# Performance work log

Hardware: AMD Instinct MI355X
Metric: run time of the kernel (lower is better)

Reference implementation:

```python
import jax, jax.numpy as jnp
import numpy as np

N_NODES = 50000
N_EDGES = 800000
IN_DIM = 128
HIDDEN = 128
LATENT = 32
BN_EPS = 1e-5


def setup_inputs() -> dict:
    key = jax.random.key(0)
    ks = jax.random.split(key, 16)
    s = 0.05
    inp = {
        "x": jax.random.normal(ks[0], (N_NODES, IN_DIM), jnp.float32),
        "edge_index": jax.random.randint(ks[1], (2, N_EDGES), 0, N_NODES),
        "edge_weight": jax.random.uniform(ks[2], (N_EDGES,), jnp.float32),
        # GCN layer 0 and 1 weights/bias
        "W0": jax.random.normal(ks[3], (IN_DIM, HIDDEN), jnp.float32) * s,
        "b0": jnp.zeros((HIDDEN,), jnp.float32),
        "W1": jax.random.normal(ks[4], (HIDDEN, HIDDEN), jnp.float32) * s,
        "b1": jnp.zeros((HIDDEN,), jnp.float32),
        # BatchNorm affine params
        "g0": jnp.ones((HIDDEN,), jnp.float32),
        "be0": jnp.zeros((HIDDEN,), jnp.float32),
        "g1": jnp.ones((HIDDEN,), jnp.float32),
        "be1": jnp.zeros((HIDDEN,), jnp.float32),
        # mean / logstd head convs
        "Wm": jax.random.normal(ks[5], (HIDDEN, LATENT), jnp.float32) * s,
        "bm": jnp.zeros((LATENT,), jnp.float32),
        "Ws": jax.random.normal(ks[6], (HIDDEN, LATENT), jnp.float32) * s,
        "bs": jnp.zeros((LATENT,), jnp.float32),
        # reparameterisation noise (materialized for determinism)
        "eps": jax.random.normal(ks[7], (N_NODES, LATENT), jnp.float32),
    }
    return inp


def _gcn_norm(edge_index, edge_weight, n):
    # add self loops with weight 1, symmetric normalization (PyG GCNConv)
    loop = jnp.arange(n)
    src = jnp.concatenate([edge_index[0], loop])
    dst = jnp.concatenate([edge_index[1], loop])
    w = jnp.concatenate([edge_weight, jnp.ones((n,), edge_weight.dtype)])
    deg = jax.ops.segment_sum(w, dst, num_segments=n)
    dinv = jnp.where(deg > 0, jax.lax.rsqrt(deg), 0.0)
    norm = dinv[src] * w * dinv[dst]
    return src, dst, norm


def _gcn(x, W, b, src, dst, norm, n):
    h = x @ W                      # [n, out]
    msg = h[src] * norm[:, None]   # gather + scale per edge
    return jax.ops.segment_sum(msg, dst, num_segments=n) + b


def _bn(x, g, b):
    m = x.mean(axis=0)
    v = x.var(axis=0)
    return (x - m) * jax.lax.rsqrt(v + BN_EPS) * g + b


def reference(x, edge_index, edge_weight, W0, b0, W1, b1, g0, be0, g1, be1,
              Wm, bm, Ws, bs, eps):
    n = x.shape[0]
    src, dst, norm = _gcn_norm(edge_index, edge_weight, n)
    # layer 0: conv -> BN -> ReLU (dropout p=0 is identity); save residual
    h = jax.nn.relu(_bn(_gcn(x, W0, b0, src, dst, norm, n), g0, be0))
    residual = h
    # layer 1
    h = jax.nn.relu(_bn(_gcn(h, W1, b1, src, dst, norm, n), g1, be1))
    h = h + residual
    q_m = _gcn(h, Wm, bm, src, dst, norm, n)
    q_s = _gcn(h, Ws, bs, src, dst, norm, n)
    std = jax.nn.softplus(q_s) + 1e-6
    q_z = q_m + std * eps  # Normal(q_m, std).rsample()
    return (q_z, q_m, q_s)
```

## Files before the change

kernel.cpp:

```cpp
#include <hip/hip_runtime.h>
#include <hip/hip_bf16.h>
#include <hip/hip_fp16.h>
#include <math.h>


#define HID 128
#define LAT 32

typedef _Float16 f16x8 __attribute__((ext_vector_type(8)));
typedef float f32x4 __attribute__((ext_vector_type(4)));

#define LOH(u) __half2float(__ushort_as_half((unsigned short)((u) & 0xFFFFu)))
#define HIH(u) __half2float(__ushort_as_half((unsigned short)((u) >> 16)))

__device__ __forceinline__ unsigned pkh(float a, float b) {
  return (unsigned)__half_as_ushort(__float2half(a)) |
         ((unsigned)__half_as_ushort(__float2half(b)) << 16);
}


__global__ __launch_bounds__(256) void k_deg_edges(const int* __restrict__ dst,
    const float* __restrict__ w, unsigned long long* __restrict__ packed,
    unsigned short* __restrict__ rank, int E) {
  int e = blockIdx.x * 256 + threadIdx.x;
  if (e < E) {
    int d = dst[e];
    unsigned long long v =
        (1ULL << 48) | (unsigned long long)(w[e] * 16777216.0f);
    unsigned long long old = atomicAdd(&packed[d], v);
    rank[e] = (unsigned short)(old >> 48);
  }
}

#define SCH 1024

__global__ __launch_bounds__(256) void k_dinv_scan(
    const unsigned long long* __restrict__ packed, float* __restrict__ dinv,
    int* __restrict__ cnt, int* __restrict__ bsum, int n) {
  int t = threadIdx.x;
  int base = blockIdx.x * SCH + t * 4;
  int s = 0;
#pragma unroll
  for (int k = 0; k < 4; ++k) {
    int i = base + k;
    if (i < n) {
      unsigned long long p = packed[i];
      int c = (int)(p >> 48);
      cnt[i] = c;
      s += c;
      float d = (float)(p & 0xFFFFFFFFFFFFULL) * (1.0f / 16777216.0f) + 1.0f;
      dinv[i] = rsqrtf(d);
    }
  }
#pragma unroll
  for (int off = 32; off; off >>= 1) s += __shfl_down(s, off);
  __shared__ int ws[4];
  if ((t & 63) == 0) ws[t >> 6] = s;
  __syncthreads();
  if (t == 0) bsum[blockIdx.x] = ws[0] + ws[1] + ws[2] + ws[3];
}

__global__ __launch_bounds__(64) void k_scan_mid(const int* __restrict__ bsum,
    int* __restrict__ boff, int* __restrict__ off, int nb, int n) {
  int t = threadIdx.x;
  int val = (t < nb) ? bsum[t] : 0;
  int inc = val;
#pragma unroll
  for (int d = 1; d < 64; d <<= 1) {
    int u = __shfl_up(inc, d);
    if (t >= d) inc += u;
  }
  if (t < nb) boff[t] = inc - val;
  if (t == nb - 1) off[n] = inc;
}

__global__ __launch_bounds__(256) void k_scan_out(const int* __restrict__ cnt,
    const int* __restrict__ boff, int* __restrict__ off, int n) {
  int base = blockIdx.x * SCH + threadIdx.x * 4;
  int4 v = make_int4(0, 0, 0, 0);
  if (base + 3 < n) v = *(const int4*)&cnt[base];
  else {
    if (base + 0 < n) v.x = cnt[base + 0];
    if (base + 1 < n) v.y = cnt[base + 1];
    if (base + 2 < n) v.z = cnt[base + 2];
  }
  int s = v.x + v.y + v.z + v.w;
  int lane = threadIdx.x & 63, wv = threadIdx.x >> 6;
  int inc = s;
#pragma unroll
  for (int d = 1; d < 64; d <<= 1) {
    int u = __shfl_up(inc, d);
    if (lane >= d) inc += u;
  }
  __shared__ int wsum[4];
  if (lane == 63) wsum[wv] = inc;
  __syncthreads();
  int wbase = 0;
  for (int i = 0; i < wv; ++i) wbase += wsum[i];
  int ex = boff[blockIdx.x] + wbase + inc - s;
  int4 o = make_int4(ex, ex + v.x, ex + v.x + v.y, ex + v.x + v.y + v.z);
  if (base + 3 < n) {
    *(int4*)&off[base] = o;
  } else {
    if (base + 0 < n) off[base + 0] = o.x;
    if (base + 1 < n) off[base + 1] = o.y;
    if (base + 2 < n) off[base + 2] = o.z;
  }
}

__global__ __launch_bounds__(256) void k_fill(const int* __restrict__ src,
    const int* __restrict__ dst, const float* __restrict__ w,
    const float* __restrict__ dinv, const int* __restrict__ coff,
    const unsigned short* __restrict__ rank, unsigned int* __restrict__ erec,
    int E) {
  int e = blockIdx.x * 256 + threadIdx.x;
  if (e < E) {
    int s = src[e], d = dst[e];
    int p = coff[d] + (int)rank[e];
    __half u = __float2half(w[e] * dinv[s]);
    erec[p] = ((unsigned)s << 16) | (unsigned)__half_as_ushort(u);
  }
}

template <int NOUT>
__global__ __launch_bounds__(256) void k_wprep(const float* __restrict__ W,
    uint4* __restrict__ Wsw) {
  int tid = blockIdx.x * 256 + threadIdx.x;
  if (tid >= (NOUT / 16) * 4 * 64) return;
  int l = tid & 63, ks = (tid >> 6) & 3, nt = tid >> 8;
  int col = nt * 16 + (l & 15);
  int kbase = ks * 32 + (l >> 4) * 8;
  _Float16 vals[8];
#pragma unroll
  for (int i = 0; i < 8; ++i) vals[i] = (_Float16)W[(kbase + i) * NOUT + col];
  Wsw[tid] = *(uint4*)vals;
}

__global__ __launch_bounds__(256) void k_wprepc(const float* __restrict__ Wm,
    const float* __restrict__ Ws, const float* __restrict__ bm,
    const float* __restrict__ bs, uint4* __restrict__ Wsw,
    float* __restrict__ bcat) {
  int tid = blockIdx.x * 256 + threadIdx.x;
  if (tid < 64) bcat[tid] = (tid < 32) ? bm[tid] : bs[tid - 32];
  if (tid >= 4 * 4 * 64) return;
  int l = tid & 63, ks = (tid >> 6) & 3, nt = tid >> 8;
  int col = nt * 16 + (l & 15);
  int kbase = ks * 32 + (l >> 4) * 8;
  const float* Wsrc = (col < 32) ? Wm : Ws;
  int c = (col < 32) ? col : col - 32;
  _Float16 vals[8];
#pragma unroll
  for (int i = 0; i < 8; ++i) vals[i] = (_Float16)Wsrc[(kbase + i) * 32 + c];
  Wsw[tid] = *(uint4*)vals;
}


#define BM 64
template <int NOUT, int MODE>
__global__ __launch_bounds__(256) void k_gemm(const void* __restrict__ Xv,
    const uint4* __restrict__ Wsw, unsigned short* __restrict__ Y, int n,
    const float* __restrict__ stats, const float* __restrict__ g,
    const float* __restrict__ be, const uint4* __restrict__ Rres,
    uint4* __restrict__ Rout) {
  constexpr int NT = NOUT / 16;
  __shared__ _Float16 xs[BM * 128];
  __shared__ float scsh[256];
  const int t = threadIdx.x;
  const int row0 = blockIdx.x * BM;
  if (MODE >= 1) {
    if (t < 128) {
      float m = stats[t] / (float)n;
      float var = fmaxf(stats[128 + t] / (float)n - m * m, 0.f);
      float sc = g[t] * rsqrtf(var + 1e-5f);
      scsh[t] = sc;
      scsh[128 + t] = be[t] - m * sc;
    }
    __syncthreads();
  }
  for (int i = t; i < BM * 16; i += 256) {
    int r = i >> 4, cg = i & 15;
    bool valid = (row0 + r) < n;
    float f[8];
    if (MODE == 0) {
      float4 v0 = make_float4(0.f, 0.f, 0.f, 0.f), v1 = v0;
      if (valid) {
        v0 = ((const float4*)Xv)[(size_t)(row0 + r) * 32 + cg * 2];
        v1 = ((const float4*)Xv)[(size_t)(row0 + r) * 32 + cg * 2 + 1];
      }
      f[0] = v0.x; f[1] = v0.y; f[2] = v0.z; f[3] = v0.w;
      f[4] = v1.x; f[5] = v1.y; f[6] = v1.z; f[7] = v1.w;
    } else {
      uint4 h = valid ? ((const uint4*)Xv)[(size_t)(row0 + r) * 16 + cg]
                      : make_uint4(0, 0, 0, 0);
      f[0] = LOH(h.x); f[1] = HIH(h.x); f[2] = LOH(h.y); f[3] = HIH(h.y);
      f[4] = LOH(h.z); f[5] = HIH(h.z); f[6] = LOH(h.w); f[7] = HIH(h.w);
    }
    if (MODE >= 1) {
      int c0 = cg * 8;
#pragma unroll
      for (int j = 0; j < 8; ++j)
        f[j] = fmaxf(f[j] * scsh[c0 + j] + scsh[128 + c0 + j], 0.f);
      if (MODE == 2 && valid) {
        uint4 rr = Rres[(size_t)(row0 + r) * 16 + cg];
        f[0] += LOH(rr.x); f[1] += HIH(rr.x);
        f[2] += LOH(rr.y); f[3] += HIH(rr.y);
        f[4] += LOH(rr.z); f[5] += HIH(rr.z);
        f[6] += LOH(rr.w); f[7] += HIH(rr.w);
      }
    }
    uint4 pk;
    pk.x = pkh(f[0], f[1]);
    pk.y = pkh(f[2], f[3]);
    pk.z = pkh(f[4], f[5]);
    pk.w = pkh(f[6], f[7]);
    if (MODE == 1 && valid) Rout[(size_t)(row0 + r) * 16 + cg] = pk;
    *(uint4*)&xs[r * 128 + ((cg ^ (r & 15)) << 3)] = pk;
  }
  __syncthreads();

  const int lane = t & 63;
  const int wave = t >> 6;
  const int arow = wave * 16 + (lane & 15);
  f16x8 a[4];
#pragma unroll
  for (int ks = 0; ks < 4; ++ks) {
    int cg = ks * 4 + (lane >> 4);
    a[ks] = *(const f16x8*)&xs[arow * 128 + ((cg ^ (arow & 15)) << 3)];
  }
  const f16x8* Wf = (const f16x8*)Wsw;
  f32x4 acc[NT];
#pragma unroll
  for (int nt = 0; nt < NT; ++nt) acc[nt] = (f32x4)(0.f);
#pragma unroll
  for (int nt = 0; nt < NT; ++nt) {
#pragma unroll
    for (int ks = 0; ks < 4; ++ks) {
      f16x8 b = Wf[(nt * 4 + ks) * 64 + lane];
      acc[nt] = __builtin_amdgcn_mfma_f32_16x16x32_f16(a[ks], b, acc[nt], 0, 0, 0);
    }
  }
  const int rbase = row0 + wave * 16 + (lane >> 4) * 4;
  const int cbase = lane & 15;
#pragma unroll
  for (int j = 0; j < 4; ++j) {
    int row = rbase + j;
    if (row < n) {
#pragma unroll
      for (int nt = 0; nt < NT; ++nt)
        Y[(size_t)row * NOUT + nt * 16 + cbase] =
            __half_as_ushort(__float2half(acc[nt][j]));
    }
  }
}

__global__ __launch_bounds__(256) void k_propb128(const uint4* __restrict__ T,
    const float* __restrict__ dinv, const int* __restrict__ off,
    const unsigned int* __restrict__ erec, const float* __restrict__ bias,
    uint4* __restrict__ outv, int n) {
  constexpr int TPN = 16;
  int node = blockIdx.x * 16 + threadIdx.x / TPN;
  int f8 = threadIdx.x % TPN;
  if (node >= n) return;
  float di = dinv[node];
  float acc[8];
  {
    uint4 v = T[(size_t)node * TPN + f8];
    acc[0] = di * LOH(v.x); acc[1] = di * HIH(v.x);
    acc[2] = di * LOH(v.y); acc[3] = di * HIH(v.y);
    acc[4] = di * LOH(v.z); acc[5] = di * HIH(v.z);
    acc[6] = di * LOH(v.w); acc[7] = di * HIH(v.w);
  }
  int e = off[node], eend = off[node + 1];
  for (; e + 1 < eend; e += 2) {
    unsigned r0 = erec[e], r1 = erec[e + 1];
    uint4 v0 = T[(size_t)(r0 >> 16) * TPN + f8];
    uint4 v1 = T[(size_t)(r1 >> 16) * TPN + f8];
    float n0 = LOH(r0), n1 = LOH(r1);
    acc[0] = fmaf(n0, LOH(v0.x), acc[0]); acc[1] = fmaf(n0, HIH(v0.x), acc[1]);
    acc[2] = fmaf(n0, LOH(v0.y), acc[2]); acc[3] = fmaf(n0, HIH(v0.y), acc[3]);
    acc[4] = fmaf(n0, LOH(v0.z), acc[4]); acc[5] = fmaf(n0, HIH(v0.z), acc[5]);
    acc[6] = fmaf(n0, LOH(v0.w), acc[6]); acc[7] = fmaf(n0, HIH(v0.w), acc[7]);
    acc[0] = fmaf(n1, LOH(v1.x), acc[0]); acc[1] = fmaf(n1, HIH(v1.x), acc[1]);
    acc[2] = fmaf(n1, LOH(v1.y), acc[2]); acc[3] = fmaf(n1, HIH(v1.y), acc[3]);
    acc[4] = fmaf(n1, LOH(v1.z), acc[4]); acc[5] = fmaf(n1, HIH(v1.z), acc[5]);
    acc[6] = fmaf(n1, LOH(v1.w), acc[6]); acc[7] = fmaf(n1, HIH(v1.w), acc[7]);
  }
  if (e < eend) {
    unsigned r0 = erec[e];
    uint4 v0 = T[(size_t)(r0 >> 16) * TPN + f8];
    float n0 = LOH(r0);
    acc[0] = fmaf(n0, LOH(v0.x), acc[0]); acc[1] = fmaf(n0, HIH(v0.x), acc[1]);
    acc[2] = fmaf(n0, LOH(v0.y), acc[2]); acc[3] = fmaf(n0, HIH(v0.y), acc[3]);
    acc[4] = fmaf(n0, LOH(v0.z), acc[4]); acc[5] = fmaf(n0, HIH(v0.z), acc[5]);
    acc[6] = fmaf(n0, LOH(v0.w), acc[6]); acc[7] = fmaf(n0, HIH(v0.w), acc[7]);
  }
  float4 b0 = *(const float4*)&bias[f8 * 8];
  float4 b1 = *(const float4*)&bias[f8 * 8 + 4];
  uint4 pk;
  pk.x = pkh(fmaf(di, acc[0], b0.x), fmaf(di, acc[1], b0.y));
  pk.y = pkh(fmaf(di, acc[2], b0.z), fmaf(di, acc[3], b0.w));
  pk.z = pkh(fmaf(di, acc[4], b1.x), fmaf(di, acc[5], b1.y));
  pk.w = pkh(fmaf(di, acc[6], b1.z), fmaf(di, acc[7], b1.w));
  outv[(size_t)node * TPN + f8] = pk;
}

__global__ __launch_bounds__(256) void k_prop64_final(const uint4* __restrict__ T,
    const float* __restrict__ dinv, const int* __restrict__ off,
    const unsigned int* __restrict__ erec, const float* __restrict__ bias,
    const float* __restrict__ eps, float* __restrict__ out, int n) {
  constexpr int TPN = 8;
  int node = blockIdx.x * 32 + threadIdx.x / TPN;
  int f8 = threadIdx.x % TPN;
  if (node >= n) return;
  float di = dinv[node];
  float acc[8];
  {
    uint4 v = T[(size_t)node * TPN + f8];
    acc[0] = di * LOH(v.x); acc[1] = di * HIH(v.x);
    acc[2] = di * LOH(v.y); acc[3] = di * HIH(v.y);
    acc[4] = di * LOH(v.z); acc[5] = di * HIH(v.z);
    acc[6] = di * LOH(v.w); acc[7] = di * HIH(v.w);
  }
  int e = off[node], eend = off[node + 1];
  for (; e + 1 < eend; e += 2) {
    unsigned r0 = erec[e], r1 = erec[e + 1];
    uint4 v0 = T[(size_t)(r0 >> 16) * TPN + f8];
    uint4 v1 = T[(size_t)(r1 >> 16) * TPN + f8];
    float n0 = LOH(r0), n1 = LOH(r1);
    acc[0] = fmaf(n0, LOH(v0.x), acc[0]); acc[1] = fmaf(n0, HIH(v0.x), acc[1]);
    acc[2] = fmaf(n0, LOH(v0.y), acc[2]); acc[3] = fmaf(n0, HIH(v0.y), acc[3]);
    acc[4] = fmaf(n0, LOH(v0.z), acc[4]); acc[5] = fmaf(n0, HIH(v0.z), acc[5]);
    acc[6] = fmaf(n0, LOH(v0.w), acc[6]); acc[7] = fmaf(n0, HIH(v0.w), acc[7]);
    acc[0] = fmaf(n1, LOH(v1.x), acc[0]); acc[1] = fmaf(n1, HIH(v1.x), acc[1]);
    acc[2] = fmaf(n1, LOH(v1.y), acc[2]); acc[3] = fmaf(n1, HIH(v1.y), acc[3]);
    acc[4] = fmaf(n1, LOH(v1.z), acc[4]); acc[5] = fmaf(n1, HIH(v1.z), acc[5]);
    acc[6] = fmaf(n1, LOH(v1.w), acc[6]); acc[7] = fmaf(n1, HIH(v1.w), acc[7]);
  }
  if (e < eend) {
    unsigned r0 = erec[e];
    uint4 v0 = T[(size_t)(r0 >> 16) * TPN + f8];
    float n0 = LOH(r0);
    acc[0] = fmaf(n0, LOH(v0.x), acc[0]); acc[1] = fmaf(n0, HIH(v0.x), acc[1]);
    acc[2] = fmaf(n0, LOH(v0.y), acc[2]); acc[3] = fmaf(n0, HIH(v0.y), acc[3]);
    acc[4] = fmaf(n0, LOH(v0.z), acc[4]); acc[5] = fmaf(n0, HIH(v0.z), acc[5]);
    acc[6] = fmaf(n0, LOH(v0.w), acc[6]); acc[7] = fmaf(n0, HIH(v0.w), acc[7]);
  }
  float4 b0 = *(const float4*)&bias[f8 * 8];
  float4 b1 = *(const float4*)&bias[f8 * 8 + 4];
  float r[8];
  r[0] = fmaf(di, acc[0], b0.x); r[1] = fmaf(di, acc[1], b0.y);
  r[2] = fmaf(di, acc[2], b0.z); r[3] = fmaf(di, acc[3], b0.w);
  r[4] = fmaf(di, acc[4], b1.x); r[5] = fmaf(di, acc[5], b1.y);
  r[6] = fmaf(di, acc[6], b1.z); r[7] = fmaf(di, acc[7], b1.w);
  float p[8];
#pragma unroll
  for (int i = 0; i < 8; ++i) p[i] = __shfl_xor(r[i], 4);
  size_t M = (size_t)n * 32;
  if (f8 < 4) {
    int jb = f8 * 8;
    float4 e0 = *(const float4*)&eps[(size_t)node * 32 + jb];
    float4 e1 = *(const float4*)&eps[(size_t)node * 32 + jb + 4];
    float ev[8] = {e0.x, e0.y, e0.z, e0.w, e1.x, e1.y, e1.z, e1.w};
    float qz[8];
#pragma unroll
    for (int i = 0; i < 8; ++i) {
      float qs = p[i];
      float sp = fmaxf(qs, 0.f) + log1pf(expf(-fabsf(qs)));
      qz[i] = fmaf(sp + 1e-6f, ev[i], r[i]);
    }
    float* oz = &out[(size_t)node * 32 + jb];
    *(float4*)oz = make_float4(qz[0], qz[1], qz[2], qz[3]);
    *(float4*)(oz + 4) = make_float4(qz[4], qz[5], qz[6], qz[7]);
    float* om = &out[M + (size_t)node * 32 + jb];
    *(float4*)om = make_float4(r[0], r[1], r[2], r[3]);
    *(float4*)(om + 4) = make_float4(r[4], r[5], r[6], r[7]);
  } else {
    int jb = (f8 - 4) * 8;
    float* os = &out[2 * M + (size_t)node * 32 + jb];
    *(float4*)os = make_float4(r[0], r[1], r[2], r[3]);
    *(float4*)(os + 4) = make_float4(r[4], r[5], r[6], r[7]);
  }
}

__global__ __launch_bounds__(256) void k_stats(const uint4* __restrict__ X4,
    float* __restrict__ stats, int n) {
  int t = threadIdx.x;
  int chunk = t & 15;
  int sub = t >> 4;
  float s[8] = {0, 0, 0, 0, 0, 0, 0, 0};
  float s2[8] = {0, 0, 0, 0, 0, 0, 0, 0};
  for (int node = blockIdx.x * 16 + sub; node < n; node += gridDim.x * 16) {
    uint4 v = X4[(size_t)node * 16 + chunk];
    float f[8] = {LOH(v.x), HIH(v.x), LOH(v.y), HIH(v.y),
                  LOH(v.z), HIH(v.z), LOH(v.w), HIH(v.w)};
#pragma unroll
    for (int i = 0; i < 8; ++i) { s[i] += f[i]; s2[i] += f[i] * f[i]; }
  }
#pragma unroll
  for (int m = 16; m <= 32; m <<= 1) {
#pragma unroll
    for (int i = 0; i < 8; ++i) {
      s[i] += __shfl_xor(s[i], m);
      s2[i] += __shfl_xor(s2[i], m);
    }
  }
  __shared__ float red[4][16][16];
  if ((t & 48) == 0) {
    int wv = t >> 6;
#pragma unroll
    for (int i = 0; i < 8; ++i) {
      red[wv][chunk][i] = s[i];
      red[wv][chunk][8 + i] = s2[i];
    }
  }
  __syncthreads();
  int c16 = t >> 4, j = t & 15;
  float v = red[0][c16][j] + red[1][c16][j] + red[2][c16][j] + red[3][c16][j];
  int col = c16 * 8 + (j & 7);
  atomicAdd(&stats[(j < 8) ? col : 128 + col], v);
}


extern "C" void kernel_launch(void* const* d_in, const int* in_sizes, int n_in,
                              void* d_out, int out_size, void* d_ws, size_t ws_size,
                              hipStream_t stream) {
  const float* x  = (const float*)d_in[0];
  const int*   ei = (const int*)d_in[1];
  const float* ew = (const float*)d_in[2];
  const float* W0 = (const float*)d_in[3];
  const float* b0 = (const float*)d_in[4];
  const float* W1 = (const float*)d_in[5];
  const float* b1 = (const float*)d_in[6];
  const float* g0 = (const float*)d_in[7];
  const float* be0 = (const float*)d_in[8];
  const float* g1 = (const float*)d_in[9];
  const float* be1 = (const float*)d_in[10];
  const float* Wm = (const float*)d_in[11];
  const float* bm = (const float*)d_in[12];
  const float* Ws = (const float*)d_in[13];
  const float* bs = (const float*)d_in[14];
  const float* eps = (const float*)d_in[15];
  float* out = (float*)d_out;

  const int n = in_sizes[0] / HID;
  const int E = in_sizes[1] / 2;
  const int* esrc = ei;
  const int* edst = ei + E;

  char* base = (char*)d_ws;
  size_t cur = 0;
  auto alloc = [&](size_t bytes) {
    size_t o = cur;
    cur = (cur + bytes + 255) & ~(size_t)255;
    return (void*)(base + o);
  };
  unsigned long long* packed = (unsigned long long*)alloc((size_t)n * 8);
  float* dinv  = (float*)alloc((size_t)n * 4);
  int*   cnt   = (int*)alloc((size_t)n * 4);
  int*   coff  = (int*)alloc((size_t)(n + 1) * 4);
  unsigned short* rank = (unsigned short*)alloc((size_t)E * 2);
  unsigned int* erec = (unsigned int*)alloc((size_t)E * 4);
  int*   bsum  = (int*)alloc(64 * 4);
  int*   boff  = (int*)alloc(64 * 4);
  float* stats0 = (float*)alloc(256 * 4);
  float* stats1 = (float*)alloc(256 * 4);
  float* bcat  = (float*)alloc(64 * 4);
  uint4* Wsw0  = (uint4*)alloc(8 * 4 * 64 * 16);
  uint4* Wsw1  = (uint4*)alloc(8 * 4 * 64 * 16);
  uint4* Wswc  = (uint4*)alloc(4 * 4 * 64 * 16);
  unsigned short* bufA = (unsigned short*)alloc((size_t)n * 128 * 2);
  unsigned short* bufB = (unsigned short*)alloc((size_t)n * 128 * 2);
  unsigned short* bufC = (unsigned short*)alloc((size_t)n * 128 * 2);
  (void)ws_size;

  const int eb = (E + 255) / 256;
  const int gemmb = (n + BM - 1) / BM;
  const int scb = (n + SCH - 1) / SCH;

  k_wprep<128><<<8, 256, 0, stream>>>(W0, Wsw0);
  k_wprep<128><<<8, 256, 0, stream>>>(W1, Wsw1);
  k_wprepc<<<4, 256, 0, stream>>>(Wm, Ws, bm, bs, Wswc, bcat);

  hipMemsetAsync(packed, 0, (size_t)n * 8, stream);
  hipMemsetAsync(stats0, 0, 256 * 4, stream);
  hipMemsetAsync(stats1, 0, 256 * 4, stream);
  k_deg_edges<<<eb, 256, 0, stream>>>(edst, ew, packed, rank, E);
  k_dinv_scan<<<scb, 256, 0, stream>>>(packed, dinv, cnt, bsum, n);
  k_scan_mid<<<1, 64, 0, stream>>>(bsum, boff, coff, scb, n);
  k_scan_out<<<scb, 256, 0, stream>>>(cnt, boff, coff, n);
  k_fill<<<eb, 256, 0, stream>>>(esrc, edst, ew, dinv, coff, rank, erec, E);

  k_gemm<128, 0><<<gemmb, 256, 0, stream>>>(x, Wsw0, bufA, n, nullptr, nullptr,
                                            nullptr, nullptr, nullptr);
  k_propb128<<<(n + 15) / 16, 256, 0, stream>>>((const uint4*)bufA, dinv, coff,
                                                erec, b0, (uint4*)bufB, n);
  k_stats<<<128, 256, 0, stream>>>((const uint4*)bufB, stats0, n);

  k_gemm<128, 1><<<gemmb, 256, 0, stream>>>(bufB, Wsw1, bufA, n, stats0, g0, be0,
                                            nullptr, (uint4*)bufC);
  k_propb128<<<(n + 15) / 16, 256, 0, stream>>>((const uint4*)bufA, dinv, coff,
                                                erec, b1, (uint4*)bufB, n);
  k_stats<<<128, 256, 0, stream>>>((const uint4*)bufB, stats1, n);

  k_gemm<64, 2><<<gemmb, 256, 0, stream>>>(bufB, Wswc, bufA, n, stats1, g1, be1,
                                           (const uint4*)bufC, nullptr);
  k_prop64_final<<<(n + 31) / 32, 256, 0, stream>>>((const uint4*)bufA, dinv,
                                                    coff, erec, bcat, eps, out, n);
}
```

Measured before the change: 230.8 us.

## Merge degree atomics with first GEMM and fold mid-scan into scan_out

Launches the edge-degree atomic kernel and the layer-0 GEMM as one grid, with block index deciding the role, so the two independent jobs overlap and one launch is removed. The tiny single-block mid-scan kernel is removed by having every scan_out block redo the 64-entry block-sum scan itself. This cuts two kernel launches and their serialization gaps. In exchange, the fused kernel carries the GEMM's shared memory footprint for every block, including the atomic-only ones, which may limit occupancy.

```diff
diff --git a/kernel.cpp b/kernel.cpp
--- a/kernel.cpp
+++ b/kernel.cpp
@@ -19,145 +19,9 @@
 }
 
 
-__global__ __launch_bounds__(256) void k_deg_edges(const int* __restrict__ dst,
-    const float* __restrict__ w, unsigned long long* __restrict__ packed,
-    unsigned short* __restrict__ rank, int E) {
-  int e = blockIdx.x * 256 + threadIdx.x;
-  if (e < E) {
-    int d = dst[e];
-    unsigned long long v =
-        (1ULL << 48) | (unsigned long long)(w[e] * 16777216.0f);
-    unsigned long long old = atomicAdd(&packed[d], v);
-    rank[e] = (unsigned short)(old >> 48);
-  }
-}
-
-#define SCH 1024
-
-__global__ __launch_bounds__(256) void k_dinv_scan(
-    const unsigned long long* __restrict__ packed, float* __restrict__ dinv,
-    int* __restrict__ cnt, int* __restrict__ bsum, int n) {
-  int t = threadIdx.x;
-  int base = blockIdx.x * SCH + t * 4;
-  int s = 0;
-#pragma unroll
-  for (int k = 0; k < 4; ++k) {
-    int i = base + k;
-    if (i < n) {
-      unsigned long long p = packed[i];
-      int c = (int)(p >> 48);
-      cnt[i] = c;
-      s += c;
-      float d = (float)(p & 0xFFFFFFFFFFFFULL) * (1.0f / 16777216.0f) + 1.0f;
-      dinv[i] = rsqrtf(d);
-    }
-  }
-#pragma unroll
-  for (int off = 32; off; off >>= 1) s += __shfl_down(s, off);
-  __shared__ int ws[4];
-  if ((t & 63) == 0) ws[t >> 6] = s;
-  __syncthreads();
-  if (t == 0) bsum[blockIdx.x] = ws[0] + ws[1] + ws[2] + ws[3];
-}
-
-__global__ __launch_bounds__(64) void k_scan_mid(const int* __restrict__ bsum,
-    int* __restrict__ boff, int* __restrict__ off, int nb, int n) {
-  int t = threadIdx.x;
-  int val = (t < nb) ? bsum[t] : 0;
-  int inc = val;
-#pragma unroll
-  for (int d = 1; d < 64; d <<= 1) {
-    int u = __shfl_up(inc, d);
-    if (t >= d) inc += u;
-  }
-  if (t < nb) boff[t] = inc - val;
-  if (t == nb - 1) off[n] = inc;
-}
-
-__global__ __launch_bounds__(256) void k_scan_out(const int* __restrict__ cnt,
-    const int* __restrict__ boff, int* __restrict__ off, int n) {
-  int base = blockIdx.x * SCH + threadIdx.x * 4;
-  int4 v = make_int4(0, 0, 0, 0);
-  if (base + 3 < n) v = *(const int4*)&cnt[base];
-  else {
-    if (base + 0 < n) v.x = cnt[base + 0];
-    if (base + 1 < n) v.y = cnt[base + 1];
-    if (base + 2 < n) v.z = cnt[base + 2];
-  }
-  int s = v.x + v.y + v.z + v.w;
-  int lane = threadIdx.x & 63, wv = threadIdx.x >> 6;
-  int inc = s;
-#pragma unroll
-  for (int d = 1; d < 64; d <<= 1) {
-    int u = __shfl_up(inc, d);
-    if (lane >= d) inc += u;
-  }
-  __shared__ int wsum[4];
-  if (lane == 63) wsum[wv] = inc;
-  __syncthreads();
-  int wbase = 0;
-  for (int i = 0; i < wv; ++i) wbase += wsum[i];
-  int ex = boff[blockIdx.x] + wbase + inc - s;
-  int4 o = make_int4(ex, ex + v.x, ex + v.x + v.y, ex + v.x + v.y + v.z);
-  if (base + 3 < n) {
-    *(int4*)&off[base] = o;
-  } else {
-    if (base + 0 < n) off[base + 0] = o.x;
-    if (base + 1 < n) off[base + 1] = o.y;
-    if (base + 2 < n) off[base + 2] = o.z;
-  }
-}
-
-__global__ __launch_bounds__(256) void k_fill(const int* __restrict__ src,
-    const int* __restrict__ dst, const float* __restrict__ w,
-    const float* __restrict__ dinv, const int* __restrict__ coff,
-    const unsigned short* __restrict__ rank, unsigned int* __restrict__ erec,
-    int E) {
-  int e = blockIdx.x * 256 + threadIdx.x;
-  if (e < E) {
-    int s = src[e], d = dst[e];
-    int p = coff[d] + (int)rank[e];
-    __half u = __float2half(w[e] * dinv[s]);
-    erec[p] = ((unsigned)s << 16) | (unsigned)__half_as_ushort(u);
-  }
-}
-
-template <int NOUT>
-__global__ __launch_bounds__(256) void k_wprep(const float* __restrict__ W,
-    uint4* __restrict__ Wsw) {
-  int tid = blockIdx.x * 256 + threadIdx.x;
-  if (tid >= (NOUT / 16) * 4 * 64) return;
-  int l = tid & 63, ks = (tid >> 6) & 3, nt = tid >> 8;
-  int col = nt * 16 + (l & 15);
-  int kbase = ks * 32 + (l >> 4) * 8;
-  _Float16 vals[8];
-#pragma unroll
-  for (int i = 0; i < 8; ++i) vals[i] = (_Float16)W[(kbase + i) * NOUT + col];
-  Wsw[tid] = *(uint4*)vals;
-}
-
-__global__ __launch_bounds__(256) void k_wprepc(const float* __restrict__ Wm,
-    const float* __restrict__ Ws, const float* __restrict__ bm,
-    const float* __restrict__ bs, uint4* __restrict__ Wsw,
-    float* __restrict__ bcat) {
-  int tid = blockIdx.x * 256 + threadIdx.x;
-  if (tid < 64) bcat[tid] = (tid < 32) ? bm[tid] : bs[tid - 32];
-  if (tid >= 4 * 4 * 64) return;
-  int l = tid & 63, ks = (tid >> 6) & 3, nt = tid >> 8;
-  int col = nt * 16 + (l & 15);
-  int kbase = ks * 32 + (l >> 4) * 8;
-  const float* Wsrc = (col < 32) ? Wm : Ws;
-  int c = (col < 32) ? col : col - 32;
-  _Float16 vals[8];
-#pragma unroll
-  for (int i = 0; i < 8; ++i) vals[i] = (_Float16)Wsrc[(kbase + i) * 32 + c];
-  Wsw[tid] = *(uint4*)vals;
-}
-
-
 #define BM 64
 template <int NOUT, int MODE>
-__global__ __launch_bounds__(256) void k_gemm(const void* __restrict__ Xv,
+__device__ __forceinline__ void gemm_dev(int bid, const void* __restrict__ Xv,
     const uint4* __restrict__ Wsw, unsigned short* __restrict__ Y, int n,
     const float* __restrict__ stats, const float* __restrict__ g,
     const float* __restrict__ be, const uint4* __restrict__ Rres,
@@ -166,7 +30,7 @@
   __shared__ _Float16 xs[BM * 128];
   __shared__ float scsh[256];
   const int t = threadIdx.x;
-  const int row0 = blockIdx.x * BM;
+  const int row0 = bid * BM;
   if (MODE >= 1) {
     if (t < 128) {
       float m = stats[t] / (float)n;
@@ -251,6 +115,160 @@
             __half_as_ushort(__float2half(acc[nt][j]));
     }
   }
+}
+
+__global__ __launch_bounds__(256) void k_front(const int* __restrict__ dst,
+    const float* __restrict__ w, unsigned long long* __restrict__ packed,
+    unsigned short* __restrict__ rank, int E, int eb,
+    const float* __restrict__ x, const uint4* __restrict__ Wsw0,
+    unsigned short* __restrict__ bufA, int n) {
+  int b = blockIdx.x;
+  if (b < eb) {
+    int e = b * 256 + threadIdx.x;
+    if (e < E) {
+      int d = dst[e];
+      unsigned long long v =
+          (1ULL << 48) | (unsigned long long)(w[e] * 16777216.0f);
+      unsigned long long old = atomicAdd(&packed[d], v);
+      rank[e] = (unsigned short)(old >> 48);
+    }
+  } else {
+    gemm_dev<128, 0>(b - eb, x, Wsw0, bufA, n, nullptr, nullptr, nullptr,
+                     nullptr, nullptr);
+  }
+}
+
+template <int NOUT, int MODE>
+__global__ __launch_bounds__(256) void k_gemm(const void* __restrict__ Xv,
+    const uint4* __restrict__ Wsw, unsigned short* __restrict__ Y, int n,
+    const float* __restrict__ stats, const float* __restrict__ g,
+    const float* __restrict__ be, const uint4* __restrict__ Rres,
+    uint4* __restrict__ Rout) {
+  gemm_dev<NOUT, MODE>(blockIdx.x, Xv, Wsw, Y, n, stats, g, be, Rres, Rout);
+}
+
+#define SCH 1024
+
+__global__ __launch_bounds__(256) void k_dinv_scan(
+    const unsigned long long* __restrict__ packed, float* __restrict__ dinv,
+    int* __restrict__ cnt, int* __restrict__ bsum, int n) {
+  int t = threadIdx.x;
+  int base = blockIdx.x * SCH + t * 4;
+  int s = 0;
+#pragma unroll
+  for (int k = 0; k < 4; ++k) {
+    int i = base + k;
+    if (i < n) {
+      unsigned long long p = packed[i];
+      int c = (int)(p >> 48);
+      cnt[i] = c;
+      s += c;
+      float d = (float)(p & 0xFFFFFFFFFFFFULL) * (1.0f / 16777216.0f) + 1.0f;
+      dinv[i] = rsqrtf(d);
+    }
+  }
+#pragma unroll
+  for (int off = 32; off; off >>= 1) s += __shfl_down(s, off);
+  __shared__ int ws[4];
+  if ((t & 63) == 0) ws[t >> 6] = s;
+  __syncthreads();
+  if (t == 0) bsum[blockIdx.x] = ws[0] + ws[1] + ws[2] + ws[3];
+}
+
+__global__ __launch_bounds__(256) void k_scan_out(const int* __restrict__ cnt,
+    const int* __restrict__ bsum, int* __restrict__ off, int nb, int n) {
+  __shared__ int sboff;
+  int t = threadIdx.x;
+  if (t < 64) {
+    int val = (t < nb) ? bsum[t] : 0;
+    int inc = val;
+#pragma unroll
+    for (int d = 1; d < 64; d <<= 1) {
+      int u = __shfl_up(inc, d);
+      if (t >= d) inc += u;
+    }
+    int exc = inc - val;
+    if (t == (int)blockIdx.x) sboff = exc;
+    if (blockIdx.x == 0 && t == nb - 1) off[n] = inc;
+  }
+  __syncthreads();
+  int boff0 = sboff;
+  int base = blockIdx.x * SCH + t * 4;
+  int4 v = make_int4(0, 0, 0, 0);
+  if (base + 3 < n) v = *(const int4*)&cnt[base];
+  else {
+    if (base + 0 < n) v.x = cnt[base + 0];
+    if (base + 1 < n) v.y = cnt[base + 1];
+    if (base + 2 < n) v.z = cnt[base + 2];
+  }
+  int s = v.x + v.y + v.z + v.w;
+  int lane = t & 63, wv = t >> 6;
+  int inc = s;
+#pragma unroll
+  for (int d = 1; d < 64; d <<= 1) {
+    int u = __shfl_up(inc, d);
+    if (lane >= d) inc += u;
+  }
+  __shared__ int wsum[4];
+  if (lane == 63) wsum[wv] = inc;
+  __syncthreads();
+  int wbase = 0;
+  for (int i = 0; i < wv; ++i) wbase += wsum[i];
+  int ex = boff0 + wbase + inc - s;
+  int4 o = make_int4(ex, ex + v.x, ex + v.x + v.y, ex + v.x + v.y + v.z);
+  if (base + 3 < n) {
+    *(int4*)&off[base] = o;
+  } else {
+    if (base + 0 < n) off[base + 0] = o.x;
+    if (base + 1 < n) off[base + 1] = o.y;
+    if (base + 2 < n) off[base + 2] = o.z;
+  }
+}
+
+__global__ __launch_bounds__(256) void k_fill(const int* __restrict__ src,
+    const int* __restrict__ dst, const float* __restrict__ w,
+    const float* __restrict__ dinv, const int* __restrict__ coff,
+    const unsigned short* __restrict__ rank, unsigned int* __restrict__ erec,
+    int E) {
+  int e = blockIdx.x * 256 + threadIdx.x;
+  if (e < E) {
+    int s = src[e], d = dst[e];
+    int p = coff[d] + (int)rank[e];
+    __half u = __float2half(w[e] * dinv[s]);
+    erec[p] = ((unsigned)s << 16) | (unsigned)__half_as_ushort(u);
+  }
+}
+
+template <int NOUT>
+__global__ __launch_bounds__(256) void k_wprep(const float* __restrict__ W,
+    uint4* __restrict__ Wsw) {
+  int tid = blockIdx.x * 256 + threadIdx.x;
+  if (tid >= (NOUT / 16) * 4 * 64) return;
+  int l = tid & 63, ks = (tid >> 6) & 3, nt = tid >> 8;
+  int col = nt * 16 + (l & 15);
+  int kbase = ks * 32 + (l >> 4) * 8;
+  _Float16 vals[8];
+#pragma unroll
+  for (int i = 0; i < 8; ++i) vals[i] = (_Float16)W[(kbase + i) * NOUT + col];
+  Wsw[tid] = *(uint4*)vals;
+}
+
+__global__ __launch_bounds__(256) void k_wprepc(const float* __restrict__ Wm,
+    const float* __restrict__ Ws, const float* __restrict__ bm,
+    const float* __restrict__ bs, uint4* __restrict__ Wsw,
+    float* __restrict__ bcat) {
+  int tid = blockIdx.x * 256 + threadIdx.x;
+  if (tid < 64) bcat[tid] = (tid < 32) ? bm[tid] : bs[tid - 32];
+  if (tid >= 4 * 4 * 64) return;
+  int l = tid & 63, ks = (tid >> 6) & 3, nt = tid >> 8;
+  int col = nt * 16 + (l & 15);
+  int kbase = ks * 32 + (l >> 4) * 8;
+  const float* Wsrc = (col < 32) ? Wm : Ws;
+  int c = (col < 32) ? col : col - 32;
+  _Float16 vals[8];
+#pragma unroll
+  for (int i = 0; i < 8; ++i) vals[i] = (_Float16)Wsrc[(kbase + i) * 32 + c];
+  Wsw[tid] = *(uint4*)vals;
 }
 
 __global__ __launch_bounds__(256) void k_propb128(const uint4* __restrict__ T,
@@ -461,7 +479,6 @@
   unsigned short* rank = (unsigned short*)alloc((size_t)E * 2);
   unsigned int* erec = (unsigned int*)alloc((size_t)E * 4);
   int*   bsum  = (int*)alloc(64 * 4);
-  int*   boff  = (int*)alloc(64 * 4);
   float* stats0 = (float*)alloc(256 * 4);
   float* stats1 = (float*)alloc(256 * 4);
   float* bcat  = (float*)alloc(64 * 4);
@@ -480,18 +497,17 @@
   k_wprep<128><<<8, 256, 0, stream>>>(W0, Wsw0);
   k_wprep<128><<<8, 256, 0, stream>>>(W1, Wsw1);
   k_wprepc<<<4, 256, 0, stream>>>(Wm, Ws, bm, bs, Wswc, bcat);
-
   hipMemsetAsync(packed, 0, (size_t)n * 8, stream);
   hipMemsetAsync(stats0, 0, 256 * 4, stream);
   hipMemsetAsync(stats1, 0, 256 * 4, stream);
-  k_deg_edges<<<eb, 256, 0, stream>>>(edst, ew, packed, rank, E);
+
+  k_front<<<eb + gemmb, 256, 0, stream>>>(edst, ew, packed, rank, E, eb,
+                                          x, Wsw0, bufA, n);
+
   k_dinv_scan<<<scb, 256, 0, stream>>>(packed, dinv, cnt, bsum, n);
-  k_scan_mid<<<1, 64, 0, stream>>>(bsum, boff, coff, scb, n);
-  k_scan_out<<<scb, 256, 0, stream>>>(cnt, boff, coff, n);
+  k_scan_out<<<scb, 256, 0, stream>>>(cnt, bsum, coff, scb, n);
   k_fill<<<eb, 256, 0, stream>>>(esrc, edst, ew, dinv, coff, rank, erec, E);
 
-  k_gemm<128, 0><<<gemmb, 256, 0, stream>>>(x, Wsw0, bufA, n, nullptr, nullptr,
-                                            nullptr, nullptr, nullptr);
   k_propb128<<<(n + 15) / 16, 256, 0, stream>>>((const uint4*)bufA, dinv, coff,
                                                 erec, b0, (uint4*)bufB, n);
   k_stats<<<128, 256, 0, stream>>>((const uint4*)bufB, stats0, n);
```

After: 224.2 us. -2.8%, faster.
